# Kernel optimization log

Measured on AMD Instinct MI355X. Metric: run time of the kernel, lower is better.

The kernel has to match this reference:

```python
import jax, jax.numpy as jnp
import numpy as np

N = 50000      # nodes
E = 1600000    # edges (avg degree 32)
F_IN = 256     # input feature dim
H = 4          # heads (layers 1,2)
C = 32         # hidden_channels
HC = H * C     # 128
NEG_SLOPE = 0.2


def setup_inputs() -> dict:
    key = jax.random.key(0)
    ks = jax.random.split(key, 18)
    def p(k, shape, scale=0.1):
        return jax.random.normal(k, shape, jnp.float32) * scale
    return {
        "x": jax.random.normal(ks[0], (N, F_IN), jnp.float32),
        "edge_index": jax.random.randint(ks[1], (2, E), 0, N),
        "edge_attr": jax.random.normal(ks[2], (E, 1), jnp.float32),
        # layer 1: 256 -> 4 heads x 32
        "W1": p(ks[3], (F_IN, HC)), "We1": p(ks[4], (1, HC)),
        "as1": p(ks[5], (H, C)), "ad1": p(ks[6], (H, C)), "ae1": p(ks[7], (H, C)),
        "b1": jnp.zeros((HC,), jnp.float32),
        # layer 2: 128 -> 4 heads x 32
        "W2": p(ks[8], (HC, HC)), "We2": p(ks[9], (1, HC)),
        "as2": p(ks[10], (H, C)), "ad2": p(ks[11], (H, C)), "ae2": p(ks[12], (H, C)),
        "b2": jnp.zeros((HC,), jnp.float32),
        # layer 3: 128 -> 1 head x 1
        "W3": p(ks[13], (HC, 1)), "We3": p(ks[14], (1, 1)),
        "as3": p(ks[15], (1, 1)), "ad3": p(ks[16], (1, 1)), "ae3": p(ks[17], (1, 1)),
        "b3": jnp.zeros((1,), jnp.float32),
    }


def _add_self_loops(edge_index, edge_attr, n):
    # PyG GATConv: add_self_loops=True, fill_value='mean' -> self-loop attr is
    # the mean of incoming edge attrs per destination node (0 if none).
    src, dst = edge_index[0], edge_index[1]
    s = jax.ops.segment_sum(edge_attr, dst, num_segments=n)
    cnt = jax.ops.segment_sum(jnp.ones((edge_attr.shape[0], 1), edge_attr.dtype), dst, num_segments=n)
    loop_attr = s / jnp.maximum(cnt, 1.0)
    ar = jnp.arange(n)
    return (jnp.concatenate([src, ar]),
            jnp.concatenate([dst, ar]),
            jnp.concatenate([edge_attr, loop_attr], axis=0))


def _gat(x, src, dst, ea, W, We, a_s, a_d, a_e, b, heads, ch, n):
    h = (x @ W).reshape(-1, heads, ch)    # [n, H, C]
    e = (ea @ We).reshape(-1, heads, ch)  # [Etot, H, C]
    ls = jnp.einsum('nhc,hc->nh', h, a_s)
    ld = jnp.einsum('nhc,hc->nh', h, a_d)
    le = jnp.einsum('ehc,hc->eh', e, a_e)
    logits = jax.nn.leaky_relu(ls[src] + ld[dst] + le, NEG_SLOPE)  # [Etot, H]
    # segment softmax over destination nodes (every node has a self-loop -> no empty segments)
    mx = jax.ops.segment_max(logits, dst, num_segments=n)
    ex = jnp.exp(logits - mx[dst])
    denom = jax.ops.segment_sum(ex, dst, num_segments=n)
    alpha = ex / (denom[dst] + 1e-16)
    out = jax.ops.segment_sum(h[src] * alpha[:, :, None], dst, num_segments=n)  # [n, H, C]
    return out.reshape(n, heads * ch) + b


def reference(x, edge_index, edge_attr,
              W1, We1, as1, ad1, ae1, b1,
              W2, We2, as2, ad2, ae2, b2,
              W3, We3, as3, ad3, ae3, b3):
    n = x.shape[0]
    src, dst, ea = _add_self_loops(edge_index, edge_attr, n)
    h = jax.nn.relu(_gat(x, src, dst, ea, W1, We1, as1, ad1, ae1, b1, H, C, n))
    h = jax.nn.relu(_gat(h, src, dst, ea, W2, We2, as2, ad2, ae2, b2, H, C, n))
    return _gat(h, src, dst, ea, W3, We3, as3, ad3, ae3, b3, 1, 1, n)  # [n, 1]
```

## Files before the change

kernel.cpp:

```cpp
#include <hip/hip_runtime.h>
#include <hip/hip_bf16.h>
#include <hip/hip_fp16.h>

#define NNODES 50000
#define NEDGES 1600000
#define ETOT   (NNODES + NEDGES)
#define FIN    256
#define HC     128
#define NEG    0.2f
#define DEGCAP 128
#define ALP    (DEGCAP + 8)

template <int K, bool XH>
__device__ __forceinline__ void gemm_body(
        const void* __restrict__ xv, const float* __restrict__ W,
        const float* __restrict__ a_s, const float* __restrict__ a_d,
        __half* __restrict__ h, float* __restrict__ ls, float* __restrict__ ld_,
        int n, int bid) {
    constexpr int BM = 64, BK = 32;
    __shared__ float xsT[BK][BM];
    __shared__ float ws[BK][HC];
    int t = threadIdx.x;
    int tx = t & 31;
    int ty = t >> 5;
    int r0 = bid * BM;

    float acc[8][4];
#pragma unroll
    for (int r = 0; r < 8; r++)
#pragma unroll
        for (int c = 0; c < 4; c++) acc[r][c] = 0.f;

    for (int kc = 0; kc < K; kc += BK) {
        __syncthreads();
#pragma unroll
        for (int q = 0; q < 2; q++) {
            int idx = q * 256 + t;
            int m = idx >> 3;
            int k4 = (idx & 7) * 4;
            int row = r0 + m;
            float vv[4] = {0.f, 0.f, 0.f, 0.f};
            if (row < n) {
                if constexpr (XH) {
                    const __half* xh = (const __half*)xv;
                    int2 rw = *(const int2*)&xh[(size_t)row * K + kc + k4];
                    float2 f0 = __half22float2(*reinterpret_cast<const __half2*>(&rw.x));
                    float2 f1 = __half22float2(*reinterpret_cast<const __half2*>(&rw.y));
                    vv[0] = f0.x; vv[1] = f0.y; vv[2] = f1.x; vv[3] = f1.y;
                } else {
                    float4 vt = *(const float4*)&((const float*)xv)[(size_t)row * K + kc + k4];
                    vv[0] = vt.x; vv[1] = vt.y; vv[2] = vt.z; vv[3] = vt.w;
                }
            }
#pragma unroll
            for (int j = 0; j < 4; j++) {
                int k = k4 + j;
                xsT[k][m ^ ((k & 7) << 2)] = vv[j];
            }
        }
#pragma unroll
        for (int q = 0; q < 4; q++) {
            int idx = q * 256 + t;
            int k = idx >> 5;
            int n4 = (idx & 31) * 4;
            *(float4*)&ws[k][n4] = *(const float4*)&W[(size_t)(kc + k) * HC + n4];
        }
        __syncthreads();
#pragma unroll
        for (int kk = 0; kk < BK; kk++) {
            int s = (kk & 7) << 2;
            float4 a0 = *(const float4*)&xsT[kk][(8 * ty) ^ s];
            float4 a1 = *(const float4*)&xsT[kk][(8 * ty + 4) ^ s];
            float4 w0 = *(const float4*)&ws[kk][4 * tx];
            float a[8] = {a0.x, a0.y, a0.z, a0.w, a1.x, a1.y, a1.z, a1.w};
            float wv[4] = {w0.x, w0.y, w0.z, w0.w};
#pragma unroll
            for (int r = 0; r < 8; r++)
#pragma unroll
                for (int c = 0; c < 4; c++)
                    acc[r][c] = fmaf(a[r], wv[c], acc[r][c]);
        }
    }

    int head = tx >> 3;
    float4 sa4 = *(const float4*)&a_s[4 * tx];
    float4 sd4 = *(const float4*)&a_d[4 * tx];
    float sa[4] = {sa4.x, sa4.y, sa4.z, sa4.w};
    float sd[4] = {sd4.x, sd4.y, sd4.z, sd4.w};
#pragma unroll
    for (int r = 0; r < 8; r++) {
        int row = r0 + 8 * ty + r;
        if (row >= n) break;
        union { __half2 h2[2]; int2 i2; } u;
        u.h2[0] = __floats2half2_rn(acc[r][0], acc[r][1]);
        u.h2[1] = __floats2half2_rn(acc[r][2], acc[r][3]);
        *(int2*)&h[(size_t)row * HC + 4 * tx] = u.i2;
        float p = acc[r][0] * sa[0] + acc[r][1] * sa[1] + acc[r][2] * sa[2] + acc[r][3] * sa[3];
        float q = acc[r][0] * sd[0] + acc[r][1] * sd[1] + acc[r][2] * sd[2] + acc[r][3] * sd[3];
        p += __shfl_xor(p, 1); q += __shfl_xor(q, 1);
        p += __shfl_xor(p, 2); q += __shfl_xor(q, 2);
        p += __shfl_xor(p, 4); q += __shfl_xor(q, 4);
        if ((tx & 7) == 0) {
            ls[row * 4 + head] = p;
            ld_[row * 4 + head] = q;
        }
    }
}

__global__ __launch_bounds__(256) void gemm1_rank_fused(
        const float* __restrict__ x, const float* __restrict__ W,
        const float* __restrict__ a_s, const float* __restrict__ a_d,
        __half* __restrict__ h, float* __restrict__ ls, float* __restrict__ ld_,
        int n,
        const int* __restrict__ ei, unsigned short* __restrict__ rank,
        int* __restrict__ deg, int E,
        const float* We1, const float* ae1, const float* We2, const float* ae2,
        const float* We3, const float* ae3, float* __restrict__ wedot,
        int gB, int rB) {
    int b = blockIdx.x;
    if (b < gB) {
        gemm_body<FIN, false>(x, W, a_s, a_d, h, ls, ld_, n, b);
    } else if (b < gB + rB) {
        int i = (b - gB) * 256 + threadIdx.x;
        if (i < E) rank[i] = (unsigned short)atomicAdd(&deg[ei[E + i]], 1);
    } else {
        int t = threadIdx.x;
        if (t < 128) {
            float p1 = We1[t] * ae1[t];
            float p2 = We2[t] * ae2[t];
            for (int o = 16; o; o >>= 1) {
                p1 += __shfl_xor(p1, o, 32);
                p2 += __shfl_xor(p2, o, 32);
            }
            if ((t & 31) == 0) {
                wedot[t >> 5] = p1;
                wedot[4 + (t >> 5)] = p2;
            }
            if (t == 0) wedot[8] = We3[0] * ae3[0];
        }
    }
}

template <int K, bool XH>
__global__ __launch_bounds__(256) void gemm_lsld(
        const void* __restrict__ x, const float* __restrict__ W,
        const float* __restrict__ a_s, const float* __restrict__ a_d,
        __half* __restrict__ h, float* __restrict__ ls, float* __restrict__ ld_,
        int n) {
    gemm_body<K, XH>(x, W, a_s, a_d, h, ls, ld_, n, blockIdx.x);
}


__global__ void scan_block(const int* __restrict__ deg, int* __restrict__ out,
                           int* __restrict__ bsum, int n) {
    __shared__ int sh[256];
    int t = threadIdx.x;
    int i = blockIdx.x * 256 + t;
    int v = (i < n) ? (deg[i] + 1) : 0;
    sh[t] = v;
    __syncthreads();
    for (int o = 1; o < 256; o <<= 1) {
        int a = (t >= o) ? sh[t - o] : 0;
        __syncthreads();
        sh[t] += a;
        __syncthreads();
    }
    if (i < n) out[i] = sh[t] - v;
    if (t == 255) bsum[blockIdx.x] = sh[255];
}

__global__ void scan_top(int* __restrict__ bsum, int nb) {
    __shared__ int sh[256];
    int t = threadIdx.x;
    int v = (t < nb) ? bsum[t] : 0;
    sh[t] = v;
    __syncthreads();
    for (int o = 1; o < 256; o <<= 1) {
        int a = (t >= o) ? sh[t - o] : 0;
        __syncthreads();
        sh[t] += a;
        __syncthreads();
    }
    if (t < nb) bsum[t] = sh[t] - v;
}

__global__ void scan_add(int* __restrict__ rp, const int* __restrict__ boff,
                         int n, int etot) {
    int i = blockIdx.x * blockDim.x + threadIdx.x;
    if (i < n)      rp[i] += boff[i >> 8];
    else if (i == n) rp[n] = etot;
}

__global__ void scatter_k(const int* __restrict__ ei, const float* __restrict__ ea,
                          const int* __restrict__ rp, const unsigned short* __restrict__ rank,
                          int2* __restrict__ csr, int E) {
    int i = blockIdx.x * blockDim.x + threadIdx.x;
    if (i < E) {
        int d = ei[E + i];
        int pos = rp[d] + (int)rank[i];
        csr[pos] = make_int2(ei[i], __float_as_int(ea[i]));
    }
}

template <bool RELU, bool FUSE3>
__global__ __launch_bounds__(128) void agg_k(
        const __half* __restrict__ h, const float* __restrict__ ls,
        const float* __restrict__ ld_, const int* __restrict__ row_ptr,
        const int2* __restrict__ csr,
        const float* __restrict__ wedot, const float* __restrict__ bias,
        __half* __restrict__ out, const float* __restrict__ W3,
        float* __restrict__ h3, int n) {
    __shared__ float albuf[4][ALP];
    __shared__ int srcbuf[DEGCAP];
    __shared__ float pacc[8][HC];
    __shared__ float hsuminv[4];
    int nid = blockIdx.x;
    int t = threadIdx.x, head = t >> 5, lane = t & 31;
    int beg = row_ptr[nid], end = row_ptr[nid + 1];
    int deg = end - beg;
    float ldn = ld_[nid * 4 + head];
    float wd = wedot[head];

    float v;
    if (deg <= DEGCAP) {
        int degr = deg - 1;
        float lgr[4];
        float mx = -1e30f, easum = 0.f;
#pragma unroll
        for (int i = 0; i < 4; i++) {
            int e = lane + 32 * i;
            float lg = -1e30f;
            if (e < degr) {
                int2 ce = csr[beg + e];
                if (head == 0) srcbuf[e] = ce.x << 8;
                float eav = __int_as_float(ce.y);
                easum += eav;
                lg = ls[ce.x * 4 + head] + ldn + eav * wd;
                lg = lg > 0.f ? lg : NEG * lg;
            }
            lgr[i] = lg;
            mx = fmaxf(mx, lg);
        }
        for (int o = 16; o; o >>= 1) {
            easum += __shfl_xor(easum, o, 32);
            mx = fmaxf(mx, __shfl_xor(mx, o, 32));
        }
        float mean = easum / fmaxf((float)degr, 1.f);
        float lgs = ls[nid * 4 + head] + ldn + mean * wd;
        lgs = lgs > 0.f ? lgs : NEG * lgs;
        mx = fmaxf(mx, lgs);

        float sum = 0.f;
#pragma unroll
        for (int i = 0; i < 4; i++) {
            int e = lane + 32 * i;
            if (e < degr) {
                float p = __expf(lgr[i] - mx);
                albuf[head][e] = p;
                sum += p;
            }
        }
        for (int o = 16; o; o >>= 1) sum += __shfl_xor(sum, o, 32);
        if (lane == 0) {
            float ps = __expf(lgs - mx);
            albuf[head][degr] = ps;
            hsuminv[head] = 1.f / (sum + ps + 1e-16f);
            if (head == 0) srcbuf[degr] = nid << 8;
        }
        __syncthreads();

        int g = t >> 4, l = t & 15;
        int c0 = 8 * l;
        const float* al = albuf[c0 >> 5];
        const char* hb = (const char*)h + 16 * l;
        float acc[8];
#pragma unroll
        for (int j = 0; j < 8; j++) acc[j] = 0.f;
        int e = g;
        for (; e + 8 < deg; e += 16) {
            int o0 = srcbuf[e], o1 = srcbuf[e + 8];
            int4 r0 = *(const int4*)(hb + o0);
            int4 r1 = *(const int4*)(hb + o1);
            float a0 = al[e], a1 = al[e + 8];
            const __half2* p0 = (const __half2*)&r0;
            const __half2* p1 = (const __half2*)&r1;
#pragma unroll
            for (int j = 0; j < 4; j++) {
                float2 f0 = __half22float2(p0[j]);
                float2 f1 = __half22float2(p1[j]);
                acc[2 * j]     = fmaf(a0, f0.x, acc[2 * j]);
                acc[2 * j + 1] = fmaf(a0, f0.y, acc[2 * j + 1]);
                acc[2 * j]     = fmaf(a1, f1.x, acc[2 * j]);
                acc[2 * j + 1] = fmaf(a1, f1.y, acc[2 * j + 1]);
            }
        }
        for (; e < deg; e += 8) {
            int o0 = srcbuf[e];
            int4 r0 = *(const int4*)(hb + o0);
            float a0 = al[e];
            const __half2* p0 = (const __half2*)&r0;
#pragma unroll
            for (int j = 0; j < 4; j++) {
                float2 f0 = __half22float2(p0[j]);
                acc[2 * j]     = fmaf(a0, f0.x, acc[2 * j]);
                acc[2 * j + 1] = fmaf(a0, f0.y, acc[2 * j + 1]);
            }
        }
#pragma unroll
        for (int j = 0; j < 4; j++)
            *(float2*)&pacc[g][c0 + 2 * j] = make_float2(acc[2 * j], acc[2 * j + 1]);
        __syncthreads();

        float inv = hsuminv[head];
        float sv = pacc[0][t];
#pragma unroll
        for (int g2 = 1; g2 < 8; g2++) sv += pacc[g2][t];
        v = sv * inv + bias[t];
    } else {
        int endr = end - 1;
        float easum = 0.f, mx = -1e30f;
        for (int j = beg + lane; j < endr; j += 32) {
            int2 ce = csr[j];
            float eav = __int_as_float(ce.y);
            easum += eav;
            float lg = ls[ce.x * 4 + head] + ldn + eav * wd;
            lg = lg > 0.f ? lg : NEG * lg;
            mx = fmaxf(mx, lg);
        }
        for (int o = 16; o; o >>= 1) {
            easum += __shfl_xor(easum, o, 32);
            mx = fmaxf(mx, __shfl_xor(mx, o, 32));
        }
        float mean = easum / fmaxf((float)(endr - beg), 1.f);
        float lgs = ls[nid * 4 + head] + ldn + mean * wd;
        lgs = lgs > 0.f ? lgs : NEG * lgs;
        mx = fmaxf(mx, lgs);
        float sum = __expf(lgs - mx);
        float acc = sum * __half2float(h[(size_t)nid * HC + t]);
        for (int j = beg; j < endr; j++) {
            int2 ce = csr[j];
            float lg = ls[ce.x * 4 + head] + ldn + __int_as_float(ce.y) * wd;
            lg = lg > 0.f ? lg : NEG * lg;
            float p = __expf(lg - mx);
            sum += p;
            acc = fmaf(p, __half2float(h[(size_t)ce.x * HC + t]), acc);
        }
        v = acc / (sum + 1e-16f) + bias[t];
        __syncthreads();
        __syncthreads();
    }

    if (RELU) v = fmaxf(v, 0.f);
    if (!FUSE3) out[(size_t)nid * HC + t] = __float2half(v);

    if (FUSE3) {
        float p = v * W3[t];
        for (int o = 32; o; o >>= 1) p += __shfl_xor(p, o, 64);
        __shared__ float sh[2];
        if ((t & 63) == 0) sh[t >> 6] = p;
        __syncthreads();
        if (t == 0) h3[nid] = sh[0] + sh[1];
    }
}

__global__ __launch_bounds__(256) void layer3_k(
        const float* __restrict__ h3, const int* __restrict__ row_ptr,
        const int2* __restrict__ csr,
        const float* __restrict__ wedot, const float* __restrict__ as3,
        const float* __restrict__ ad3, const float* __restrict__ b3,
        float* __restrict__ out, int n) {
    int idx = blockIdx.x * blockDim.x + threadIdx.x;
    int node = idx >> 3, l = idx & 7;
    if (node >= n) return;
    float A = as3[0], D = ad3[0], wd = wedot[8];
    int beg = row_ptr[node], endr = row_ptr[node + 1] - 1;
    float hs = h3[node];
    float hdn = hs * D;

    float easum = 0.f, mx = -1e30f;
    for (int j = beg + l; j < endr; j += 8) {
        int2 ce = csr[j];
        float eav = __int_as_float(ce.y);
        easum += eav;
        float lg = h3[ce.x] * A + hdn + eav * wd;
        lg = lg > 0.f ? lg : NEG * lg;
        mx = fmaxf(mx, lg);
    }
    easum += __shfl_xor(easum, 1, 8); mx = fmaxf(mx, __shfl_xor(mx, 1, 8));
    easum += __shfl_xor(easum, 2, 8); mx = fmaxf(mx, __shfl_xor(mx, 2, 8));
    easum += __shfl_xor(easum, 4, 8); mx = fmaxf(mx, __shfl_xor(mx, 4, 8));
    float mean = easum / fmaxf((float)(endr - beg), 1.f);
    float lgs = hs * A + hdn + mean * wd;
    lgs = lgs > 0.f ? lgs : NEG * lgs;
    mx = fmaxf(mx, lgs);

    float sum = 0.f, num = 0.f;
    for (int j = beg + l; j < endr; j += 8) {
        int2 ce = csr[j];
        float hv = h3[ce.x];
        float lg = hv * A + hdn + __int_as_float(ce.y) * wd;
        lg = lg > 0.f ? lg : NEG * lg;
        float p = __expf(lg - mx);
        sum += p;
        num = fmaf(p, hv, num);
    }
    sum += __shfl_xor(sum, 1, 8); num += __shfl_xor(num, 1, 8);
    sum += __shfl_xor(sum, 2, 8); num += __shfl_xor(num, 2, 8);
    sum += __shfl_xor(sum, 4, 8); num += __shfl_xor(num, 4, 8);
    if (l == 0) {
        float p = __expf(lgs - mx);
        sum += p;
        num = fmaf(p, hs, num);
        out[node] = num / (sum + 1e-16f) + b3[0];
    }
}


extern "C" void kernel_launch(void* const* d_in, const int* in_sizes, int n_in,
                              void* d_out, int out_size, void* d_ws, size_t ws_size,
                              hipStream_t stream) {
    const float* x   = (const float*)d_in[0];
    const int*   ei  = (const int*)d_in[1];
    const float* ea  = (const float*)d_in[2];
    const float* W1  = (const float*)d_in[3];
    const float* We1 = (const float*)d_in[4];
    const float* as1 = (const float*)d_in[5];
    const float* ad1 = (const float*)d_in[6];
    const float* ae1 = (const float*)d_in[7];
    const float* b1  = (const float*)d_in[8];
    const float* W2  = (const float*)d_in[9];
    const float* We2 = (const float*)d_in[10];
    const float* as2 = (const float*)d_in[11];
    const float* ad2 = (const float*)d_in[12];
    const float* ae2 = (const float*)d_in[13];
    const float* b2  = (const float*)d_in[14];
    const float* W3  = (const float*)d_in[15];
    const float* We3 = (const float*)d_in[16];
    const float* as3 = (const float*)d_in[17];
    const float* ad3 = (const float*)d_in[18];
    const float* ae3 = (const float*)d_in[19];
    const float* b3  = (const float*)d_in[20];

    const int N = NNODES, E = NEDGES, etot = ETOT;

    char* ws = (char*)d_ws;
    size_t o = 0;
    auto alloc = [&](size_t bytes) { size_t r = o; o = (o + bytes + 255) & ~(size_t)255; return r; };
    size_t o_deg   = alloc((size_t)N * 4);
    size_t zero_span = o;
    size_t o_rp    = alloc((size_t)(N + 1) * 4);
    size_t o_bsum  = alloc(256 * 4);
    size_t o_wd    = alloc(16 * 4);
    size_t o_rank  = alloc((size_t)E * 2);
    size_t o_csr   = alloc((size_t)etot * 8);
    size_t o_ls    = alloc((size_t)N * 4 * 4);
    size_t o_ld    = alloc((size_t)N * 4 * 4);
    size_t o_h3    = alloc((size_t)N * 4);
    size_t o_h16   = alloc((size_t)N * HC * 2);
    size_t o_h16b  = alloc((size_t)N * HC * 2);

    int*            deg   = (int*)(ws + o_deg);
    int*            rp    = (int*)(ws + o_rp);
    int*            bsum  = (int*)(ws + o_bsum);
    float*          wd    = (float*)(ws + o_wd);
    unsigned short* rank  = (unsigned short*)(ws + o_rank);
    int2*           csr   = (int2*)(ws + o_csr);
    float*          ls    = (float*)(ws + o_ls);
    float*          ld_   = (float*)(ws + o_ld);
    float*          h3    = (float*)(ws + o_h3);
    __half*         h16   = (__half*)(ws + o_h16);
    __half*         h16b  = (__half*)(ws + o_h16b);

    hipMemsetAsync(ws, 0, zero_span, stream);

    int gB = (N + 63) / 64;
    int rB = (E + 255) / 256;
    int nb = (N + 255) / 256;

    gemm1_rank_fused<<<gB + rB + 1, 256, 0, stream>>>(
        x, W1, as1, ad1, h16, ls, ld_, N,
        ei, rank, deg, E,
        We1, ae1, We2, ae2, We3, ae3, wd, gB, rB);

    scan_block<<<nb, 256, 0, stream>>>(deg, rp, bsum, N);
    scan_top<<<1, 256, 0, stream>>>(bsum, nb);
    scan_add<<<(N + 256) / 256, 256, 0, stream>>>(rp, bsum, N, etot);
    scatter_k<<<(E + 255) / 256, 256, 0, stream>>>(ei, ea, rp, rank, csr, E);

    agg_k<true, false><<<N, 128, 0, stream>>>(h16, ls, ld_, rp, csr, wd, b1,
                                              h16b, nullptr, nullptr, N);
    gemm_lsld<HC, true><<<(N + 63) / 64, 256, 0, stream>>>(h16b, W2, as2, ad2,
                                                           h16, ls, ld_, N);
    agg_k<true, true><<<N, 128, 0, stream>>>(h16, ls, ld_, rp, csr, wd + 4, b2,
                                             nullptr, W3, h3, N);
    layer3_k<<<(N * 8 + 255) / 256, 256, 0, stream>>>(h3, rp, csr, wd, as3, ad3, b3,
                                                      (float*)d_out, N);
}
```

Baseline: 301.9 us.

## Use fp16 packed dot2 in GEMM inner loop with templated row tile

Converts the x and W tiles to packed fp16 pairs in shared memory and computes the GEMM with v_dot2 (fdot2) instructions accumulating in fp32, which halves the number of FMA-type instructions and the LDS footprint. The row tile is made a template parameter, and the layer-2 GEMM uses 32-row blocks to launch more blocks. Rounding the fp32 input x and the weights to fp16 reduces accuracy in layer 1, and the shared-memory swizzle is replaced by padding.

```diff
diff --git a/kernel.cpp b/kernel.cpp
--- a/kernel.cpp
+++ b/kernel.cpp
@@ -11,30 +11,42 @@
 #define DEGCAP 128
 #define ALP    (DEGCAP + 8)
 
-template <int K, bool XH>
+typedef _Float16 h2 __attribute__((ext_vector_type(2)));
+
+__device__ __forceinline__ float fdot2f(h2 a, h2 b, float c) {
+#if __has_builtin(__builtin_amdgcn_fdot2)
+    return __builtin_amdgcn_fdot2(a, b, c, false);
+#else
+    return fmaf((float)a.x, (float)b.x, fmaf((float)a.y, (float)b.y, c));
+#endif
+}
+
+template <int K, int BM, bool XH>
 __device__ __forceinline__ void gemm_body(
         const void* __restrict__ xv, const float* __restrict__ W,
         const float* __restrict__ a_s, const float* __restrict__ a_d,
         __half* __restrict__ h, float* __restrict__ ls, float* __restrict__ ld_,
         int n, int bid) {
-    constexpr int BM = 64, BK = 32;
-    __shared__ float xsT[BK][BM];
-    __shared__ float ws[BK][HC];
+    constexpr int BK = 32;
+    constexpr int BKH = BK / 2;
+    constexpr int RM = BM / 8;
+    __shared__ h2 xA[BKH][BM + 2];
+    __shared__ h2 wW[BKH][HC];
     int t = threadIdx.x;
     int tx = t & 31;
     int ty = t >> 5;
     int r0 = bid * BM;
 
-    float acc[8][4];
-#pragma unroll
-    for (int r = 0; r < 8; r++)
+    float acc[RM][4];
+#pragma unroll
+    for (int r = 0; r < RM; r++)
 #pragma unroll
         for (int c = 0; c < 4; c++) acc[r][c] = 0.f;
 
     for (int kc = 0; kc < K; kc += BK) {
         __syncthreads();
 #pragma unroll
-        for (int q = 0; q < 2; q++) {
+        for (int q = 0; q < BM / 32; q++) {
             int idx = q * 256 + t;
             int m = idx >> 3;
             int k4 = (idx & 7) * 4;
@@ -52,33 +64,42 @@
                     vv[0] = vt.x; vv[1] = vt.y; vv[2] = vt.z; vv[3] = vt.w;
                 }
             }
-#pragma unroll
-            for (int j = 0; j < 4; j++) {
-                int k = k4 + j;
-                xsT[k][m ^ ((k & 7) << 2)] = vv[j];
-            }
-        }
-#pragma unroll
-        for (int q = 0; q < 4; q++) {
+            int j0 = k4 >> 1;
+            h2 p0, p1;
+            p0.x = (_Float16)vv[0]; p0.y = (_Float16)vv[1];
+            p1.x = (_Float16)vv[2]; p1.y = (_Float16)vv[3];
+            xA[j0][m] = p0;
+            xA[j0 + 1][m] = p1;
+        }
+#pragma unroll
+        for (int q = 0; q < 2; q++) {
             int idx = q * 256 + t;
-            int k = idx >> 5;
-            int n4 = (idx & 31) * 4;
-            *(float4*)&ws[k][n4] = *(const float4*)&W[(size_t)(kc + k) * HC + n4];
-        }
-        __syncthreads();
-#pragma unroll
-        for (int kk = 0; kk < BK; kk++) {
-            int s = (kk & 7) << 2;
-            float4 a0 = *(const float4*)&xsT[kk][(8 * ty) ^ s];
-            float4 a1 = *(const float4*)&xsT[kk][(8 * ty + 4) ^ s];
-            float4 w0 = *(const float4*)&ws[kk][4 * tx];
-            float a[8] = {a0.x, a0.y, a0.z, a0.w, a1.x, a1.y, a1.z, a1.w};
-            float wv[4] = {w0.x, w0.y, w0.z, w0.w};
-#pragma unroll
-            for (int r = 0; r < 8; r++)
-#pragma unroll
-                for (int c = 0; c < 4; c++)
-                    acc[r][c] = fmaf(a[r], wv[c], acc[r][c]);
+            int j = idx >> 5;
+            int c4 = (idx & 31) * 4;
+            float4 w0 = *(const float4*)&W[(size_t)(kc + 2 * j) * HC + c4];
+            float4 w1 = *(const float4*)&W[(size_t)(kc + 2 * j + 1) * HC + c4];
+            h2 a, b, c, d;
+            a.x = (_Float16)w0.x; a.y = (_Float16)w1.x;
+            b.x = (_Float16)w0.y; b.y = (_Float16)w1.y;
+            c.x = (_Float16)w0.z; c.y = (_Float16)w1.z;
+            d.x = (_Float16)w0.w; d.y = (_Float16)w1.w;
+            wW[j][c4] = a; wW[j][c4 + 1] = b; wW[j][c4 + 2] = c; wW[j][c4 + 3] = d;
+        }
+        __syncthreads();
+#pragma unroll
+        for (int j = 0; j < BKH; j++) {
+            h2 a[RM];
+#pragma unroll
+            for (int r = 0; r < RM; r++) a[r] = xA[j][RM * ty + r];
+            h2 w0 = wW[j][4 * tx], w1 = wW[j][4 * tx + 1];
+            h2 w2 = wW[j][4 * tx + 2], w3 = wW[j][4 * tx + 3];
+#pragma unroll
+            for (int r = 0; r < RM; r++) {
+                acc[r][0] = fdot2f(a[r], w0, acc[r][0]);
+                acc[r][1] = fdot2f(a[r], w1, acc[r][1]);
+                acc[r][2] = fdot2f(a[r], w2, acc[r][2]);
+                acc[r][3] = fdot2f(a[r], w3, acc[r][3]);
+            }
         }
     }
 
@@ -88,12 +109,12 @@
     float sa[4] = {sa4.x, sa4.y, sa4.z, sa4.w};
     float sd[4] = {sd4.x, sd4.y, sd4.z, sd4.w};
 #pragma unroll
-    for (int r = 0; r < 8; r++) {
-        int row = r0 + 8 * ty + r;
+    for (int r = 0; r < RM; r++) {
+        int row = r0 + RM * ty + r;
         if (row >= n) break;
-        union { __half2 h2[2]; int2 i2; } u;
-        u.h2[0] = __floats2half2_rn(acc[r][0], acc[r][1]);
-        u.h2[1] = __floats2half2_rn(acc[r][2], acc[r][3]);
+        union { __half2 h2v[2]; int2 i2; } u;
+        u.h2v[0] = __floats2half2_rn(acc[r][0], acc[r][1]);
+        u.h2v[1] = __floats2half2_rn(acc[r][2], acc[r][3]);
         *(int2*)&h[(size_t)row * HC + 4 * tx] = u.i2;
         float p = acc[r][0] * sa[0] + acc[r][1] * sa[1] + acc[r][2] * sa[2] + acc[r][3] * sa[3];
         float q = acc[r][0] * sd[0] + acc[r][1] * sd[1] + acc[r][2] * sd[2] + acc[r][3] * sd[3];
@@ -119,7 +140,7 @@
         int gB, int rB) {
     int b = blockIdx.x;
     if (b < gB) {
-        gemm_body<FIN, false>(x, W, a_s, a_d, h, ls, ld_, n, b);
+        gemm_body<FIN, 64, false>(x, W, a_s, a_d, h, ls, ld_, n, b);
     } else if (b < gB + rB) {
         int i = (b - gB) * 256 + threadIdx.x;
         if (i < E) rank[i] = (unsigned short)atomicAdd(&deg[ei[E + i]], 1);
@@ -141,13 +162,13 @@
     }
 }
 
-template <int K, bool XH>
+template <int K, int BM, bool XH>
 __global__ __launch_bounds__(256) void gemm_lsld(
         const void* __restrict__ x, const float* __restrict__ W,
         const float* __restrict__ a_s, const float* __restrict__ a_d,
         __half* __restrict__ h, float* __restrict__ ls, float* __restrict__ ld_,
         int n) {
-    gemm_body<K, XH>(x, W, a_s, a_d, h, ls, ld_, n, blockIdx.x);
+    gemm_body<K, BM, XH>(x, W, a_s, a_d, h, ls, ld_, n, blockIdx.x);
 }
 
 
@@ -489,8 +510,8 @@
 
     agg_k<true, false><<<N, 128, 0, stream>>>(h16, ls, ld_, rp, csr, wd, b1,
                                               h16b, nullptr, nullptr, N);
-    gemm_lsld<HC, true><<<(N + 63) / 64, 256, 0, stream>>>(h16b, W2, as2, ad2,
-                                                           h16, ls, ld_, N);
+    gemm_lsld<HC, 32, true><<<(N + 31) / 32, 256, 0, stream>>>(h16b, W2, as2, ad2,
+                                                               h16, ls, ld_, N);
     agg_k<true, true><<<N, 128, 0, stream>>>(h16, ls, ld_, rp, csr, wd + 4, b2,
                                              nullptr, W3, h3, N);
     layer3_k<<<(N * 8 + 255) / 256, 256, 0, stream>>>(h3, rp, csr, wd, as3, ad3, b3,
```

Result: no change. 296.2 us (-1.9%).
